# Optimization experiments

Measured on AMD Instinct MI355X. Metric: run time of the kernel, lower is better.

The kernel has to match this reference:

```python
import jax, jax.numpy as jnp
import numpy as np

MIN_STD = 0.01
FOURIER_SCALE = 20.0


def _grid_sample_bilinear(h_flat, gx, gy):
    """Bilinear grid_sample with align_corners=True.
    h_flat: (N, C, H, W); gx, gy: (N, P) in [-1, 1].
    Returns (N, P, C)."""
    N, C, H, W = h_flat.shape
    x = (gx + 1.0) * 0.5 * (W - 1)
    y = (gy + 1.0) * 0.5 * (H - 1)
    x0 = jnp.clip(jnp.floor(x), 0, W - 1)
    y0 = jnp.clip(jnp.floor(y), 0, H - 1)
    x1 = jnp.clip(x0 + 1, 0, W - 1)
    y1 = jnp.clip(y0 + 1, 0, H - 1)
    wx = x - x0
    wy = y - y0
    x0i, x1i = x0.astype(jnp.int32), x1.astype(jnp.int32)
    y0i, y1i = y0.astype(jnp.int32), y1.astype(jnp.int32)
    hf = h_flat.reshape(N, C, H * W)  # flatten spatial for gather

    def gather(yi, xi):
        idx = (yi * W + xi)[:, None, :]  # (N,1,P)
        return jnp.take_along_axis(hf, idx, axis=2)  # (N,C,P)

    v00 = gather(y0i, x0i)
    v01 = gather(y0i, x1i)
    v10 = gather(y1i, x0i)
    v11 = gather(y1i, x1i)
    wx_ = wx[:, None, :]
    wy_ = wy[:, None, :]
    top = v00 * (1 - wx_) + v01 * wx_
    bot = v10 * (1 - wx_) + v11 * wx_
    out = top * (1 - wy_) + bot * wy_  # (N,C,P)
    return out.transpose(0, 2, 1)  # (N,P,C)


def setup_inputs() -> dict:
    key = jax.random.key(0)
    ks = jax.random.split(key, 9)
    B, T, C, Hg, Wg, P = 8, 16, 128, 64, 64, 2048
    h_dim, fmap = 128, 128
    in_dim = h_dim + 2 * fmap  # 384
    h_grid = jax.random.normal(ks[0], (B, T, C, Hg, Wg), dtype=jnp.float32)
    xs = jax.random.uniform(ks[1], (B, T, P, 1), dtype=jnp.float32)
    ys = jax.random.uniform(ks[2], (B, T, P, 1), dtype=jnp.float32)
    B_mat = jax.random.normal(ks[3], (2, fmap), dtype=jnp.float32) * FOURIER_SCALE
    W0 = jax.random.normal(ks[4], (in_dim, h_dim), dtype=jnp.float32) / np.sqrt(in_dim)
    b0 = jnp.zeros((h_dim,), dtype=jnp.float32)
    W1 = jax.random.normal(ks[5], (h_dim, h_dim), dtype=jnp.float32) / np.sqrt(h_dim)
    b1 = jnp.zeros((h_dim,), dtype=jnp.float32)
    W2 = jax.random.normal(ks[6], (h_dim, 2), dtype=jnp.float32) / np.sqrt(h_dim)
    b2 = jnp.zeros((2,), dtype=jnp.float32)
    return {"h_grid": h_grid, "xs": xs, "ys": ys, "B_mat": B_mat,
            "W0": W0, "b0": b0, "W1": W1, "b1": b1, "W2": W2, "b2": b2}


def reference(h_grid, xs, ys, B_mat, W0, b0, W1, b1, W2, b2):
    B, T, P, _ = xs.shape
    _, _, C, Hg, Wg = h_grid.shape
    h_flat = h_grid.reshape(B * T, C, Hg, Wg)
    coords = jnp.concatenate([xs, ys], axis=-1).reshape(B * T, P, 2)
    # map [spatial_min, spatial_max]=[0,1] to [-1,1]
    g = 2.0 * coords - 1.0
    sampled = _grid_sample_bilinear(h_flat, g[..., 0], g[..., 1])  # (BT,P,C)
    # Fourier features: [sin(2pi x B), cos(2pi x B)]
    proj = 2.0 * jnp.pi * jnp.einsum('npd,df->npf', coords, B_mat)
    spatial = jnp.concatenate([jnp.sin(proj), jnp.cos(proj)], axis=-1)  # (BT,P,256)
    x = jnp.concatenate([sampled, spatial], axis=-1)  # (BT,P,384)
    x = jax.nn.relu(x @ W0 + b0)
    x = jax.nn.relu(x @ W1 + b1)
    out = (x @ W2 + b2).reshape(B, T, P, 2)
    mu = out[..., 0:1]
    sigma = jax.nn.softplus(out[..., 1:2]) + MIN_STD
    return jnp.concatenate([mu, sigma], axis=-1)  # (B,T,P,2)
```

## Files before the change

kernel.cpp:

```cpp
#include <hip/hip_runtime.h>
#include <hip/hip_bf16.h>
#include <math.h>

typedef __attribute__((ext_vector_type(8))) short short8;
typedef __attribute__((ext_vector_type(4))) float f32x4;

__device__ __forceinline__ float b2f(unsigned short u) {
    union { unsigned int i; float f; } v; v.i = ((unsigned int)u) << 16; return v.f;
}
__device__ __forceinline__ unsigned short f2b(float f) {
    __hip_bfloat16 h = __float2bfloat16(f);
    return *reinterpret_cast<unsigned short*>(&h);
}

__global__ __launch_bounds__(256) void transpose_h(const float* __restrict__ hg,
                                                   unsigned short* __restrict__ ht) {
    __shared__ float t[64][65];
    int bid = blockIdx.x;
    int n  = bid >> 7;
    int cb = (bid >> 6) & 1;
    int pb = bid & 63;
    int tid = threadIdx.x;
    int j = tid & 63, i0 = tid >> 6;
    const float* src = hg + ((size_t)(n * 128 + cb * 64)) * 4096 + pb * 64;
#pragma unroll
    for (int ii = 0; ii < 16; ++ii) {
        int i = i0 + ii * 4;
        t[i][j] = src[(size_t)i * 4096 + j];
    }
    __syncthreads();
    int c = tid & 63, j0 = tid >> 6;
    unsigned short* dst = ht + ((size_t)n * 4096 + pb * 64) * 128 + cb * 64 + c;
#pragma unroll
    for (int jj = 0; jj < 16; ++jj) {
        int jr = j0 + jj * 4;
        dst[(size_t)jr * 128] = f2b(t[c][jr]);
    }
}

__global__ void prep_weights(const float* __restrict__ W0, const float* __restrict__ W1,
                             unsigned short* __restrict__ w0t, unsigned short* __restrict__ w1t) {
    int i = blockIdx.x * 256 + threadIdx.x;
    const int total0 = 128 * 384, total1 = 128 * 128;
    for (int idx = i; idx < total0; idx += gridDim.x * 256) {
        int j = idx / 384, k = idx - j * 384;
        w0t[idx] = f2b(W0[k * 128 + j]);
    }
    for (int idx = i; idx < total1; idx += gridDim.x * 256) {
        int j = idx >> 7, k = idx & 127;
        w1t[idx] = f2b(W1[k * 128 + j]);
    }
}

#define HSTR 136

#define MFMA_BF16 __builtin_amdgcn_mfma_f32_16x16x32_bf16

__global__ __launch_bounds__(256) void fused_decoder(
    const unsigned short* __restrict__ ht,
    const float* __restrict__ xs, const float* __restrict__ ys,
    const float* __restrict__ Bm,
    const unsigned short* __restrict__ w0t, const float* __restrict__ b0,
    const unsigned short* __restrict__ w1t, const float* __restrict__ b1,
    const float* __restrict__ W2, const float* __restrict__ b2,
    float* __restrict__ out)
{
    __shared__ unsigned short hb_all[4 * 16 * HSTR];
    __shared__ unsigned short w2l[256];

    int tid = threadIdx.x, lane = tid & 63, w = tid >> 6;
    int lr = lane & 15, lg = lane >> 4;
    unsigned short* hb = hb_all + w * 16 * HSTR;

    { int o = tid >> 7, k = tid & 127; w2l[o * 128 + k] = f2b(W2[k * 2 + o]); }
    __syncthreads();

    int bid = blockIdx.x;
    int swz = (bid & 7) * 256 + (bid >> 3);
    int n = swz >> 4;
    int pb = (swz & 15) * 128 + w * 32;
    int gp0 = n * 2048 + pb;

    float xm[2], ym[2], wxv[2], wyv[2];
    int o00[2], o01[2], o10[2], o11[2];
#pragma unroll
    for (int m = 0; m < 2; ++m) {
        int gp = gp0 + m * 16 + lr;
        float x = xs[gp], y = ys[gp];
        xm[m] = x; ym[m] = y;
        float px = x * 63.f, py = y * 63.f;
        float x0f = fminf(fmaxf(floorf(px), 0.f), 63.f);
        float y0f = fminf(fmaxf(floorf(py), 0.f), 63.f);
        wxv[m] = px - x0f; wyv[m] = py - y0f;
        int xi0 = (int)x0f, yi0 = (int)y0f;
        int xi1 = min(xi0 + 1, 63), yi1 = min(yi0 + 1, 63);
        o00[m] = (yi0 * 64 + xi0) * 256;
        o01[m] = (yi0 * 64 + xi1) * 256;
        o10[m] = (yi1 * 64 + xi0) * 256;
        o11[m] = (yi1 * 64 + xi1) * 256;
    }
    const char* base = (const char*)ht + ((size_t)n << 20) + lg * 16;

    f32x4 acc[2][8];
#pragma unroll
    for (int nj = 0; nj < 8; ++nj) {
        float bv = b0[nj * 16 + lr];
        acc[0][nj] = (f32x4){bv, bv, bv, bv};
        acc[1][nj] = acc[0][nj];
    }

    short8 c00[2], c01[2], c10[2], c11[2];
#pragma unroll
    for (int m = 0; m < 2; ++m) {
        c00[m] = *(const short8*)(base + o00[m]);
        c01[m] = *(const short8*)(base + o01[m]);
        c10[m] = *(const short8*)(base + o10[m]);
        c11[m] = *(const short8*)(base + o11[m]);
    }

#pragma unroll
    for (int s = 0; s < 4; ++s) {
        int f0 = s * 32 + lg * 8;
        f32x4 B0a = *(const f32x4*)&Bm[f0];
        f32x4 B0b = *(const f32x4*)&Bm[f0 + 4];
        f32x4 B1a = *(const f32x4*)&Bm[128 + f0];
        f32x4 B1b = *(const f32x4*)&Bm[128 + f0 + 4];
        short8 asn[2], acs[2];
#pragma unroll
        for (int m = 0; m < 2; ++m) {
            float t_[8];
#pragma unroll
            for (int j = 0; j < 4; ++j) {
                t_[j]     = xm[m] * B0a[j] + ym[m] * B1a[j];
                t_[4 + j] = xm[m] * B0b[j] + ym[m] * B1b[j];
            }
#pragma unroll
            for (int j = 0; j < 8; ++j) {
                float tf = t_[j] - floorf(t_[j]);
                float sv, cv;
                asm("v_sin_f32 %0, %1" : "=v"(sv) : "v"(tf));
                asm("v_cos_f32 %0, %1" : "=v"(cv) : "v"(tf));
                asn[m][j] = (short)f2b(sv);
                acs[m][j] = (short)f2b(cv);
            }
        }
        int kss = 4 + s, ksc = 8 + s;
#pragma unroll
        for (int nj = 0; nj < 8; ++nj) {
            short8 bs = *(const short8*)&w0t[(nj * 16 + lr) * 384 + kss * 32 + lg * 8];
            acc[0][nj] = MFMA_BF16(asn[0], bs, acc[0][nj], 0, 0, 0);
            acc[1][nj] = MFMA_BF16(asn[1], bs, acc[1][nj], 0, 0, 0);
        }
#pragma unroll
        for (int nj = 0; nj < 8; ++nj) {
            short8 bc = *(const short8*)&w0t[(nj * 16 + lr) * 384 + ksc * 32 + lg * 8];
            acc[0][nj] = MFMA_BF16(acs[0], bc, acc[0][nj], 0, 0, 0);
            acc[1][nj] = MFMA_BF16(acs[1], bc, acc[1][nj], 0, 0, 0);
        }

        short8 a[2];
#pragma unroll
        for (int m = 0; m < 2; ++m) {
            float wx = wxv[m], wy = wyv[m];
            float ivx = 1.f - wx, ivy = 1.f - wy;
#pragma unroll
            for (int j = 0; j < 8; ++j) {
                float top = b2f((unsigned short)c00[m][j]) * ivx + b2f((unsigned short)c01[m][j]) * wx;
                float bot = b2f((unsigned short)c10[m][j]) * ivx + b2f((unsigned short)c11[m][j]) * wx;
                a[m][j] = (short)f2b(top * ivy + bot * wy);
            }
        }
        if (s < 3) {
            int so = (s + 1) * 64;
#pragma unroll
            for (int m = 0; m < 2; ++m) {
                c00[m] = *(const short8*)(base + o00[m] + so);
                c01[m] = *(const short8*)(base + o01[m] + so);
                c10[m] = *(const short8*)(base + o10[m] + so);
                c11[m] = *(const short8*)(base + o11[m] + so);
            }
        }
#pragma unroll
        for (int nj = 0; nj < 8; ++nj) {
            short8 b = *(const short8*)&w0t[(nj * 16 + lr) * 384 + s * 32 + lg * 8];
            acc[0][nj] = MFMA_BF16(a[0], b, acc[0][nj], 0, 0, 0);
            acc[1][nj] = MFMA_BF16(a[1], b, acc[1][nj], 0, 0, 0);
        }
    }

    short8 a1[2][4];
#pragma unroll
    for (int m = 0; m < 2; ++m) {
#pragma unroll
        for (int nj = 0; nj < 8; ++nj)
#pragma unroll
            for (int r = 0; r < 4; ++r)
                hb[(lg * 4 + r) * HSTR + nj * 16 + lr] = f2b(fmaxf(acc[m][nj][r], 0.f));
        asm volatile("s_waitcnt lgkmcnt(0)" ::: "memory");
#pragma unroll
        for (int ks = 0; ks < 4; ++ks)
            a1[m][ks] = *(const short8*)&hb[lr * HSTR + ks * 32 + lg * 8];
        asm volatile("s_waitcnt lgkmcnt(0)" ::: "memory");
    }
#pragma unroll
    for (int nj = 0; nj < 8; ++nj) {
        float bv = b1[nj * 16 + lr];
        acc[0][nj] = (f32x4){bv, bv, bv, bv};
        acc[1][nj] = acc[0][nj];
    }
#pragma unroll
    for (int ks = 0; ks < 4; ++ks)
#pragma unroll
        for (int nj = 0; nj < 8; ++nj) {
            short8 b = *(const short8*)&w1t[(nj * 16 + lr) * 128 + ks * 32 + lg * 8];
            acc[0][nj] = MFMA_BF16(a1[0][ks], b, acc[0][nj], 0, 0, 0);
            acc[1][nj] = MFMA_BF16(a1[1][ks], b, acc[1][nj], 0, 0, 0);
        }

    float bb2 = (lr < 2) ? b2[lr] : 0.f;
#pragma unroll
    for (int m = 0; m < 2; ++m) {
#pragma unroll
        for (int nj = 0; nj < 8; ++nj)
#pragma unroll
            for (int r = 0; r < 4; ++r)
                hb[(lg * 4 + r) * HSTR + nj * 16 + lr] = f2b(fmaxf(acc[m][nj][r], 0.f));
        asm volatile("s_waitcnt lgkmcnt(0)" ::: "memory");
        f32x4 acc2 = (f32x4){bb2, bb2, bb2, bb2};
#pragma unroll
        for (int ks = 0; ks < 4; ++ks) {
            short8 a2 = *(const short8*)&hb[lr * HSTR + ks * 32 + lg * 8];
            short8 bz = (short8){0, 0, 0, 0, 0, 0, 0, 0};
            if (lr < 2) bz = *(const short8*)&w2l[lr * 128 + ks * 32 + lg * 8];
            acc2 = MFMA_BF16(a2, bz, acc2, 0, 0, 0);
        }
        asm volatile("s_waitcnt lgkmcnt(0)" ::: "memory");
        if (lr < 2) {
#pragma unroll
            for (int r = 0; r < 4; ++r) {
                int gp = gp0 + m * 16 + lg * 4 + r;
                float v = acc2[r];
                if (lr == 0) {
                    out[gp * 2] = v;
                } else {
                    float sp = (v > 20.f) ? v : log1pf(expf(v));
                    out[gp * 2 + 1] = sp + 0.01f;
                }
            }
        }
    }
}

extern "C" void kernel_launch(void* const* d_in, const int* in_sizes, int n_in,
                              void* d_out, int out_size, void* d_ws, size_t ws_size,
                              hipStream_t stream) {
    const float* h_grid = (const float*)d_in[0];
    const float* xs = (const float*)d_in[1];
    const float* ys = (const float*)d_in[2];
    const float* Bm = (const float*)d_in[3];
    const float* W0 = (const float*)d_in[4];
    const float* b0 = (const float*)d_in[5];
    const float* W1 = (const float*)d_in[6];
    const float* b1 = (const float*)d_in[7];
    const float* W2 = (const float*)d_in[8];
    const float* b2 = (const float*)d_in[9];
    float* out = (float*)d_out;

    unsigned short* ht  = (unsigned short*)d_ws;
    unsigned short* w0t = (unsigned short*)((char*)d_ws + 134217728ull);
    unsigned short* w1t = w0t + 128 * 384;

    hipLaunchKernelGGL(transpose_h, dim3(16384), dim3(256), 0, stream, h_grid, ht);
    hipLaunchKernelGGL(prep_weights, dim3(64), dim3(256), 0, stream, W0, W1, w0t, w1t);
    hipLaunchKernelGGL(fused_decoder, dim3(2048), dim3(256), 0, stream,
                       ht, xs, ys, Bm, w0t, b0, w1t, b1, W2, b2, out);
}
```

Baseline: 247.0 us.

## Stage W0 in XOR-swizzled LDS and double block size to 512 threads

Result: faster. 210.7 us (-14.7%).

```diff
diff --git a/kernel.cpp b/kernel.cpp
--- a/kernel.cpp
+++ b/kernel.cpp
@@ -53,10 +53,13 @@
 }
 
 #define HSTR 136
-
 #define MFMA_BF16 __builtin_amdgcn_mfma_f32_16x16x32_bf16
 
-__global__ __launch_bounds__(256) void fused_decoder(
+__device__ __forceinline__ const short8* w0frag(const unsigned short* w0s, int row, int kb) {
+    return (const short8*)((const char*)w0s + row * 768 + (kb ^ ((row & 7) << 4)));
+}
+
+__global__ __launch_bounds__(512, 2) void fused_decoder(
     const unsigned short* __restrict__ ht,
     const float* __restrict__ xs, const float* __restrict__ ys,
     const float* __restrict__ Bm,
@@ -65,21 +68,33 @@
     const float* __restrict__ W2, const float* __restrict__ b2,
     float* __restrict__ out)
 {
-    __shared__ unsigned short hb_all[4 * 16 * HSTR];
+    __shared__ unsigned short w0s[128 * 384];
+    __shared__ unsigned short hb_all[8 * 16 * HSTR];
     __shared__ unsigned short w2l[256];
 
     int tid = threadIdx.x, lane = tid & 63, w = tid >> 6;
     int lr = lane & 15, lg = lane >> 4;
     unsigned short* hb = hb_all + w * 16 * HSTR;
 
-    { int o = tid >> 7, k = tid & 127; w2l[o * 128 + k] = f2b(W2[k * 2 + o]); }
+    {
+        const short8* src = (const short8*)w0t;
+#pragma unroll
+        for (int it = 0; it < 12; ++it) {
+            int c = tid + it * 512;
+            int row = c / 48;
+            int wb = (c - row * 48) * 16;
+            short8 v = src[c];
+            *(short8*)((char*)w0s + row * 768 + (wb ^ ((row & 7) << 4))) = v;
+        }
+        if (tid < 256) { int o = tid >> 7, k = tid & 127; w2l[o * 128 + k] = f2b(W2[k * 2 + o]); }
+    }
     __syncthreads();
 
     int bid = blockIdx.x;
-    int swz = (bid & 7) * 256 + (bid >> 3);
-    int n = swz >> 4;
-    int pb = (swz & 15) * 128 + w * 32;
-    int gp0 = n * 2048 + pb;
+    int swz = (bid & 7) * 128 + (bid >> 3);
+    int n = swz >> 3;
+    int pbw = (swz & 7) * 256 + w * 32;
+    int gp0 = n * 2048 + pbw;
 
     float xm[2], ym[2], wxv[2], wyv[2];
     int o00[2], o01[2], o10[2], o11[2];
@@ -144,16 +159,16 @@
                 acs[m][j] = (short)f2b(cv);
             }
         }
-        int kss = 4 + s, ksc = 8 + s;
-#pragma unroll
-        for (int nj = 0; nj < 8; ++nj) {
-            short8 bs = *(const short8*)&w0t[(nj * 16 + lr) * 384 + kss * 32 + lg * 8];
+        int kbs = (4 + s) * 64 + lg * 16, kbc = (8 + s) * 64 + lg * 16;
+#pragma unroll
+        for (int nj = 0; nj < 8; ++nj) {
+            short8 bs = *w0frag(w0s, nj * 16 + lr, kbs);
             acc[0][nj] = MFMA_BF16(asn[0], bs, acc[0][nj], 0, 0, 0);
             acc[1][nj] = MFMA_BF16(asn[1], bs, acc[1][nj], 0, 0, 0);
         }
 #pragma unroll
         for (int nj = 0; nj < 8; ++nj) {
-            short8 bc = *(const short8*)&w0t[(nj * 16 + lr) * 384 + ksc * 32 + lg * 8];
+            short8 bc = *w0frag(w0s, nj * 16 + lr, kbc);
             acc[0][nj] = MFMA_BF16(acs[0], bc, acc[0][nj], 0, 0, 0);
             acc[1][nj] = MFMA_BF16(acs[1], bc, acc[1][nj], 0, 0, 0);
         }
@@ -180,9 +195,10 @@
                 c11[m] = *(const short8*)(base + o11[m] + so);
             }
         }
-#pragma unroll
-        for (int nj = 0; nj < 8; ++nj) {
-            short8 b = *(const short8*)&w0t[(nj * 16 + lr) * 384 + s * 32 + lg * 8];
+        int kba = s * 64 + lg * 16;
+#pragma unroll
+        for (int nj = 0; nj < 8; ++nj) {
+            short8 b = *w0frag(w0s, nj * 16 + lr, kba);
             acc[0][nj] = MFMA_BF16(a[0], b, acc[0][nj], 0, 0, 0);
             acc[1][nj] = MFMA_BF16(a[1], b, acc[1][nj], 0, 0, 0);
         }
@@ -272,6 +288,6 @@
 
     hipLaunchKernelGGL(transpose_h, dim3(16384), dim3(256), 0, stream, h_grid, ht);
     hipLaunchKernelGGL(prep_weights, dim3(64), dim3(256), 0, stream, W0, W1, w0t, w1t);
-    hipLaunchKernelGGL(fused_decoder, dim3(2048), dim3(256), 0, stream,
+    hipLaunchKernelGGL(fused_decoder, dim3(1024), dim3(512), 0, stream,
                        ht, xs, ys, Bm, w0t, b0, w1t, b1, W2, b2, out);
 }
```
